# Optimization experiments

Hardware: AMD Instinct MI355X
Metric: run time of the kernel (lower is better)

The kernel has to match this reference:

```python
import jax, jax.numpy as jnp
import numpy as np
import math

DIMS = [2048, 1024, 512, 4096]
NH, DK, DV = 16, 64, 64
BS = 8192
D_MODEL = NH * DK  # 1024


def setup_inputs() -> dict:
    key = jax.random.key(0)
    ks = jax.random.split(key, 3 * len(DIMS) + 5)
    inp = {"input_data": jax.random.normal(ks[0], (BS, sum(DIMS)), jnp.float32)}
    ki = 1
    for i, d in enumerate(DIMS):
        inp[f"wq{i}"] = jax.random.normal(ks[ki], (NH * DK, d), jnp.float32) * 0.02; ki += 1
        inp[f"wk{i}"] = jax.random.normal(ks[ki], (NH * DK, d), jnp.float32) * 0.02; ki += 1
        inp[f"wv{i}"] = jax.random.normal(ks[ki], (NH * DV, d), jnp.float32) * 0.02; ki += 1
    inp["fc_w"] = jax.random.normal(ks[ki], (NH * DV, NH * DV), jnp.float32) * 0.02; ki += 1
    inp["fc_b"] = jax.random.normal(ks[ki], (NH * DV,), jnp.float32) * 0.02; ki += 1
    inp["ln_g"] = jnp.ones((NH * DV,), jnp.float32)
    inp["ln_b"] = jnp.zeros((NH * DV,), jnp.float32)
    return inp


def _forward(input_data, wqs, wks, wvs, fc_w, fc_b, ln_g, ln_b):
    bs = input_data.shape[0]
    M = len(DIMS)
    offs = np.cumsum([0] + DIMS)
    # per-modality projections; stack into [bs, M, NH*D]
    xs = [input_data[:, offs[i]:offs[i + 1]] for i in range(M)]
    q = jnp.stack([x @ w.T for x, w in zip(xs, wqs)], axis=1)  # [bs, M, NH*DK]
    k = jnp.stack([x @ w.T for x, w in zip(xs, wks)], axis=1)
    v = jnp.stack([x @ w.T for x, w in zip(xs, wvs)], axis=1)  # [bs, M, NH*DV]
    residual = v  # v.transpose(1,2).view == original stacked v
    qh = q.reshape(bs, M, NH, DK).transpose(0, 2, 1, 3)  # [bs, NH, M, DK]
    kh = k.reshape(bs, M, NH, DK).transpose(0, 2, 1, 3)
    vh = v.reshape(bs, M, NH, DV).transpose(0, 2, 1, 3)
    scores = jnp.einsum('bhqd,bhkd->bhqk', qh, kh) / math.sqrt(DK)
    attn = jax.nn.softmax(scores, axis=-1)  # [bs, NH, M, M]
    ctx = jnp.einsum('bhqk,bhkd->bhqd', attn, vh)  # [bs, NH, M, DV]
    ctx = ctx.transpose(0, 2, 1, 3).reshape(bs, M, NH * DV)
    out = ctx @ fc_w.T + fc_b  # dropout is identity (p=0 / eval)
    out = out + residual
    mu = jnp.mean(out, axis=-1, keepdims=True)
    var = jnp.var(out, axis=-1, keepdims=True)
    out = (out - mu) / jnp.sqrt(var + 1e-6) * ln_g + ln_b
    return out, attn


def reference(input_data, wq0, wk0, wv0, wq1, wk1, wv1, wq2, wk2, wv2,
              wq3, wk3, wv3, fc_w, fc_b, ln_g, ln_b):
    wqs = [wq0, wq1, wq2, wq3]
    wks = [wk0, wk1, wk2, wk3]
    wvs = [wv0, wv1, wv2, wv3]
    return _forward(input_data, wqs, wks, wvs, fc_w, fc_b, ln_g, ln_b)
```

## Files before the change

### kernel.cpp

```cpp
#include <hip/hip_runtime.h>


typedef unsigned short u16;
typedef short short8 __attribute__((ext_vector_type(8)));
typedef float f32x4 __attribute__((ext_vector_type(4)));

__device__ __forceinline__ u16 f2bf(float f) {
  unsigned u = __builtin_bit_cast(unsigned, f);
  u += 0x7FFFu + ((u >> 16) & 1u);
  return (u16)(u >> 16);
}
__device__ __forceinline__ float bf2f(u16 s) {
  return __builtin_bit_cast(float, ((unsigned)s) << 16);
}

__device__ __forceinline__ void gload16(const u16* g, u16* l) {
  __builtin_amdgcn_global_load_lds(
      (const __attribute__((address_space(1))) void*)g,
      (__attribute__((address_space(3))) void*)l, 16, 0, 0);
}

#define CFENCE asm volatile("" ::: "memory")

struct CArgs {
  const float* src[14];
  unsigned long dst[14];
  int blk0[14];
  int n4[14];
};

__global__ __launch_bounds__(256) void convall(CArgs a, u16* __restrict__ wsb) {
  int blk = blockIdx.x;
  int s = 0;
#pragma unroll
  for (int i = 1; i < 14; ++i) s = (blk >= a.blk0[i]) ? i : s;
  int li = (blk - a.blk0[s]) * 256 + threadIdx.x;
  if (li < a.n4[s]) {
    float4 v = ((const float4*)a.src[s])[li];
    ushort4 o;
    o.x = f2bf(v.x); o.y = f2bf(v.y); o.z = f2bf(v.z); o.w = f2bf(v.w);
    ((ushort4*)(wsb + a.dst[s]))[li] = o;
  }
}

template <int MODE>
__global__ __launch_bounds__(512, 2)
void gemm8(const u16* __restrict__ Abase, int lda,
           const u16* __restrict__ Wbase, u16* __restrict__ Cq,
           u16* __restrict__ Cpre, const float* __restrict__ bias,
           const u16* __restrict__ resid) {
  __shared__ __align__(16) u16 lds[65536];

  const int tid = threadIdx.x;
  const int w = tid >> 6, lane = tid & 63;
  const int lr = lane & 15, lk = lane >> 4;
  const int wm = w >> 2, wn = w & 3;

  int K, nt, bx, by, coff;
  const u16 *A, *B;
  if (MODE == 0) {
    int seg = blockIdx.x / 384;
    int r = blockIdx.x % 384;
    bx = r % 12; by = r / 12;
    K = 4096 >> seg; nt = 64 >> seg;
    int xo, wo, mod;
    switch (seg) {
      case 0:  xo = 3584; wo = 11010048; mod = 3; break;
      case 1:  xo = 0;    wo = 0;        mod = 0; break;
      case 2:  xo = 2048; wo = 6291456;  mod = 1; break;
      default: xo = 3072; wo = 9437184;  mod = 2; break;
    }
    coff = mod * 3072;
    A = Abase + xo;
    B = Wbase + wo;
  } else {
    bx = blockIdx.x & 3; by = blockIdx.x >> 2;
    K = 1024; nt = 16; coff = 0;
    A = Abase; B = Wbase;
  }
  const size_t brow = (size_t)by * 256;
  const int bcol = bx * 256;
  const u16* Ab = A + brow * (size_t)lda;
  const u16* Bb = B + (size_t)bcol * (size_t)K;

  f32x4 acc[8][4];
#pragma unroll
  for (int i = 0; i < 8; ++i)
#pragma unroll
    for (int j = 0; j < 4; ++j) acc[i][j] = (f32x4){0.f, 0.f, 0.f, 0.f};

  auto stageA = [&](int p, int half) {
    const int base = (p & 1) * 65536 + half * 16384;
    const int k0 = p * 64;
#pragma unroll
    for (int l = 0; l < 2; ++l) {
      int s = l * 8192 + tid * 16;
      int rw = s >> 7;
      int ck = ((s >> 4) & 7) ^ (rw & 7);
      int row = (rw & 63) + ((rw >> 6) << 7) + half * 64;
      gload16(Ab + (size_t)row * lda + k0 + ck * 8, &lds[(base + s) >> 1]);
    }
  };
  auto stageB = [&](int p, int half) {
    const int base = (p & 1) * 65536 + 32768 + half * 16384;
    const int k0 = p * 64;
#pragma unroll
    for (int l = 0; l < 2; ++l) {
      int s = l * 8192 + tid * 16;
      int rw = s >> 7;
      int ck = ((s >> 4) & 7) ^ (rw & 7);
      int col = (rw & 31) + ((rw >> 5) << 6) + half * 32;
      gload16(Bb + (size_t)col * (size_t)K + k0 + ck * 8, &lds[(base + s) >> 1]);
    }
  };

  auto ldA = [&](int t, int half, short8* dst) {
    const u16* lp = lds + (((t & 1) * 65536 + half * 16384) >> 1);
#pragma unroll
    for (int mi = 0; mi < 4; ++mi) {
      int rw = mi * 16 + lr + wm * 64;
#pragma unroll
      for (int ks = 0; ks < 2; ++ks) {
        int pc = (ks * 4 + lk) ^ (rw & 7);
        dst[mi * 2 + ks] = *(const short8*)(lp + rw * 64 + pc * 8);
      }
    }
  };
  auto ldB = [&](int t, int half, short8* dst) {
    const u16* lp = lds + (((t & 1) * 65536 + 32768 + half * 16384) >> 1);
#pragma unroll
    for (int ni = 0; ni < 2; ++ni) {
      int rw = ni * 16 + lr + wn * 32;
#pragma unroll
      for (int ks = 0; ks < 2; ++ks) {
        int pc = (ks * 4 + lk) ^ (rw & 7);
        dst[ni * 2 + ks] = *(const short8*)(lp + rw * 64 + pc * 8);
      }
    }
  };

  short8 af[8], bl[4], bh[4];
  auto MQ = [&](short8* a, short8* b, int mo, int no) {
#pragma unroll
    for (int mi = 0; mi < 4; ++mi)
#pragma unroll
      for (int ni = 0; ni < 2; ++ni) {
        acc[mo + mi][no + ni] = __builtin_amdgcn_mfma_f32_16x16x32_bf16(
            a[mi * 2 + 0], b[ni * 2 + 0], acc[mo + mi][no + ni], 0, 0, 0);
        acc[mo + mi][no + ni] = __builtin_amdgcn_mfma_f32_16x16x32_bf16(
            a[mi * 2 + 1], b[ni * 2 + 1], acc[mo + mi][no + ni], 0, 0, 0);
      }
  };

  stageA(0, 0); stageB(0, 0); stageB(0, 1); stageA(0, 1);
  asm volatile("s_waitcnt vmcnt(4)" ::: "memory");
  __builtin_amdgcn_s_barrier();
  CFENCE;

#pragma unroll 1
  for (int t = 0; t < nt; ++t) {
    const bool more = (t + 1 < nt);
    ldA(t, 0, af);
    ldB(t, 0, bl);
    if (more) stageA(t + 1, 0);
    CFENCE;
    __builtin_amdgcn_s_barrier();
    asm volatile("s_waitcnt lgkmcnt(0)" ::: "memory");
    __builtin_amdgcn_sched_barrier(0);
    __builtin_amdgcn_s_setprio(1);
    MQ(af, bl, 0, 0);
    __builtin_amdgcn_s_setprio(0);
    CFENCE;
    if (more) asm volatile("s_waitcnt vmcnt(4)" ::: "memory");
    else      asm volatile("s_waitcnt vmcnt(2)" ::: "memory");
    __builtin_amdgcn_s_barrier();
    CFENCE;
    ldB(t, 1, bh);
    if (more) stageB(t + 1, 0);
    CFENCE;
    __builtin_amdgcn_s_barrier();
    asm volatile("s_waitcnt lgkmcnt(0)" ::: "memory");
    __builtin_amdgcn_sched_barrier(0);
    __builtin_amdgcn_s_setprio(1);
    MQ(af, bh, 0, 2);
    __builtin_amdgcn_s_setprio(0);
    CFENCE;
    if (more) asm volatile("s_waitcnt vmcnt(4)" ::: "memory");
    else      asm volatile("s_waitcnt vmcnt(0)" ::: "memory");
    __builtin_amdgcn_s_barrier();
    CFENCE;
    ldA(t, 1, af);
    if (more) stageB(t + 1, 1);
    CFENCE;
    __builtin_amdgcn_s_barrier();
    asm volatile("s_waitcnt lgkmcnt(0)" ::: "memory");
    __builtin_amdgcn_sched_barrier(0);
    __builtin_amdgcn_s_setprio(1);
    MQ(af, bh, 4, 2);
    __builtin_amdgcn_s_setprio(0);
    CFENCE;
    __builtin_amdgcn_s_barrier();
    CFENCE;
    if (more) stageA(t + 1, 1);
    CFENCE;
    __builtin_amdgcn_s_barrier();
    __builtin_amdgcn_s_setprio(1);
    MQ(af, bl, 4, 0);
    __builtin_amdgcn_s_setprio(0);
    CFENCE;
    if (more) {
      asm volatile("s_waitcnt vmcnt(4)" ::: "memory");
      __builtin_amdgcn_s_barrier();
      CFENCE;
    }
  }

  if (MODE == 0) {
#pragma unroll
    for (int mi = 0; mi < 8; ++mi)
#pragma unroll
      for (int ni = 0; ni < 4; ++ni) {
        const int c = coff + bcol + wn * 64 + ni * 16 + lr;
#pragma unroll
        for (int j = 0; j < 4; ++j) {
          size_t r = brow + wm * 128 + mi * 16 + lk * 4 + j;
          Cq[r * 12288 + c] = f2bf(acc[mi][ni][j]);
        }
      }
  } else {
#pragma unroll
    for (int mi = 0; mi < 8; ++mi)
#pragma unroll
      for (int ni = 0; ni < 4; ++ni) {
        const int c = bcol + wn * 64 + ni * 16 + lr;
        const float bs = bias[c];
#pragma unroll
        for (int j = 0; j < 4; ++j) {
          size_t r = brow + wm * 128 + mi * 16 + lk * 4 + j;
          size_t ridx = (r >> 2) * 12288 + (r & 3) * 3072 + 2048 + c;
          Cpre[r * 1024 + c] = f2bf(acc[mi][ni][j] + bs + bf2f(resid[ridx]));
        }
      }
  }
}

__global__ __launch_bounds__(256) void attn_k(const u16* __restrict__ qkv,
                                              u16* __restrict__ ctxb,
                                              float* __restrict__ attn_out) {
  const int tid = threadIdx.x;
  const int l = tid & 63;
  const int wg = blockIdx.x * 4 + (tid >> 6);
  const int b = wg >> 2;
  const int h0 = (wg & 3) << 2;
  const size_t base = (size_t)b * 12288 + h0 * 64 + l * 4;

  float q[4][4], k[4][4], v[4][4];
#pragma unroll
  for (int m = 0; m < 4; ++m) {
    ushort4 uq = *(const ushort4*)(qkv + base + m * 3072);
    ushort4 uk = *(const ushort4*)(qkv + base + m * 3072 + 1024);
    ushort4 uv = *(const ushort4*)(qkv + base + m * 3072 + 2048);
    q[m][0] = bf2f(uq.x); q[m][1] = bf2f(uq.y); q[m][2] = bf2f(uq.z); q[m][3] = bf2f(uq.w);
    k[m][0] = bf2f(uk.x); k[m][1] = bf2f(uk.y); k[m][2] = bf2f(uk.z); k[m][3] = bf2f(uk.w);
    v[m][0] = bf2f(uv.x); v[m][1] = bf2f(uv.y); v[m][2] = bf2f(uv.z); v[m][3] = bf2f(uv.w);
  }

  float s[16];
#pragma unroll
  for (int i = 0; i < 4; ++i)
#pragma unroll
    for (int j = 0; j < 4; ++j) {
      float acc = q[i][0] * k[j][0];
      acc += q[i][1] * k[j][1];
      acc += q[i][2] * k[j][2];
      acc += q[i][3] * k[j][3];
      s[i * 4 + j] = acc;
    }
#pragma unroll
  for (int off = 1; off < 16; off <<= 1) {
#pragma unroll
    for (int t = 0; t < 16; ++t) s[t] += __shfl_xor(s[t], off);
  }

  float a[16];
#pragma unroll
  for (int i = 0; i < 4; ++i) {
    float s0 = s[i * 4 + 0] * 0.125f, s1 = s[i * 4 + 1] * 0.125f;
    float s2 = s[i * 4 + 2] * 0.125f, s3 = s[i * 4 + 3] * 0.125f;
    float m = fmaxf(fmaxf(s0, s1), fmaxf(s2, s3));
    float e0 = __expf(s0 - m), e1 = __expf(s1 - m);
    float e2 = __expf(s2 - m), e3 = __expf(s3 - m);
    float inv = 1.0f / (e0 + e1 + e2 + e3);
    a[i * 4 + 0] = e0 * inv; a[i * 4 + 1] = e1 * inv;
    a[i * 4 + 2] = e2 * inv; a[i * 4 + 3] = e3 * inv;
  }

#pragma unroll
  for (int i = 0; i < 4; ++i) {
    float c0 = a[i*4+0]*v[0][0] + a[i*4+1]*v[1][0] + a[i*4+2]*v[2][0] + a[i*4+3]*v[3][0];
    float c1 = a[i*4+0]*v[0][1] + a[i*4+1]*v[1][1] + a[i*4+2]*v[2][1] + a[i*4+3]*v[3][1];
    float c2 = a[i*4+0]*v[0][2] + a[i*4+1]*v[1][2] + a[i*4+2]*v[2][2] + a[i*4+3]*v[3][2];
    float c3 = a[i*4+0]*v[0][3] + a[i*4+1]*v[1][3] + a[i*4+2]*v[2][3] + a[i*4+3]*v[3][3];
    ushort4 o;
    o.x = f2bf(c0); o.y = f2bf(c1); o.z = f2bf(c2); o.w = f2bf(c3);
    *(ushort4*)(ctxb + (size_t)b * 4096 + i * 1024 + h0 * 64 + l * 4) = o;
  }

  int sel = l & 15;
  float val = a[0];
#pragma unroll
  for (int t = 1; t < 16; ++t) val = (sel == t) ? a[t] : val;
  attn_out[(size_t)b * 256 + h0 * 16 + l] = val;
}

__global__ __launch_bounds__(256) void ln_k(const u16* __restrict__ pre,
                                            const float* __restrict__ g,
                                            const float* __restrict__ b,
                                            float* __restrict__ out) {
  int row = blockIdx.x;
  int tid = threadIdx.x;
  ushort4 u = *(const ushort4*)(pre + (size_t)row * 1024 + tid * 4);
  float x0 = bf2f(u.x), x1 = bf2f(u.y), x2 = bf2f(u.z), x3 = bf2f(u.w);
  float s = x0 + x1 + x2 + x3;
  float s2 = x0 * x0 + x1 * x1 + x2 * x2 + x3 * x3;
#pragma unroll
  for (int off = 32; off; off >>= 1) {
    s += __shfl_xor(s, off);
    s2 += __shfl_xor(s2, off);
  }
  __shared__ float r1[4], r2[4];
  int w = tid >> 6, lane = tid & 63;
  if (lane == 0) { r1[w] = s; r2[w] = s2; }
  __syncthreads();
  s = r1[0] + r1[1] + r1[2] + r1[3];
  s2 = r2[0] + r2[1] + r2[2] + r2[3];
  float mu = s * (1.0f / 1024.0f);
  float inv = rsqrtf(s2 * (1.0f / 1024.0f) - mu * mu + 1e-6f);
  float4 gv = *(const float4*)(g + tid * 4);
  float4 bv = *(const float4*)(b + tid * 4);
  float4 o;
  o.x = (x0 - mu) * inv * gv.x + bv.x;
  o.y = (x1 - mu) * inv * gv.y + bv.y;
  o.z = (x2 - mu) * inv * gv.z + bv.z;
  o.w = (x3 - mu) * inv * gv.w + bv.w;
  *(float4*)(out + (size_t)row * 1024 + tid * 4) = o;
}

extern "C" void kernel_launch(void* const* d_in, const int* in_sizes, int n_in,
                              void* d_out, int out_size, void* d_ws,
                              size_t ws_size, hipStream_t stream) {
  const float* fcb = (const float*)d_in[14];
  const float* lng = (const float*)d_in[15];
  const float* lnb = (const float*)d_in[16];

  u16* wsb = (u16*)d_ws;
  u16* xb = wsb;
  u16* wb = xb + 62914560;
  u16* qkv = wb + 24641536;
  u16* ctxb = qkv + 100663296;
  u16* pre = wsb;
  float* outp = (float*)d_out;
  float* attn_out = outp + 33554432;

  static const unsigned long woff[13] = {
      0,        2097152,  4194304,
      6291456,  7340032,  8388608,
      9437184,  9961472,  10485760,
      11010048, 15204352, 19398656,
      23592960};
  static const int wn4[13] = {524288, 524288, 524288, 262144, 262144, 262144,
                              131072, 131072, 131072, 1048576, 1048576, 1048576,
                              262144};

  CArgs ca;
  ca.src[0] = (const float*)d_in[0];
  ca.dst[0] = 0;
  ca.n4[0] = 62914560 / 4;
  ca.blk0[0] = 0;
  int nb = ca.n4[0] / 256;
  for (int i = 0; i < 13; ++i) {
    ca.src[i + 1] = (const float*)d_in[1 + i];
    ca.dst[i + 1] = 62914560ul + woff[i];
    ca.n4[i + 1] = wn4[i];
    ca.blk0[i + 1] = nb;
    nb += (wn4[i] + 255) / 256;
  }
  convall<<<dim3(nb), 256, 0, stream>>>(ca, wsb);

  gemm8<0><<<dim3(1536), 512, 0, stream>>>(xb, 7680, wb, qkv, nullptr, nullptr,
                                           nullptr);

  attn_k<<<dim3(8192), 256, 0, stream>>>(qkv, ctxb, attn_out);

  gemm8<1><<<dim3(512), 512, 0, stream>>>(ctxb, 1024, wb + 23592960, nullptr,
                                          pre, fcb, qkv);

  ln_k<<<dim3(32768), 256, 0, stream>>>(pre, lng, lnb, outp);
}
```

Baseline: 617.0 us.

## Use nontemporal loads/stores in streaming kernels and regroup GEMM prefetch stages

Streaming accesses in the conversion, attention and layernorm kernels become nontemporal loads and stores so single-use data does not pollute the caches. The GEMM main loop now issues the next tile's A and B prefetches in two grouped batches instead of four separate points. This removes one barrier and one wait per iteration. The regrouping changes how many loads are in flight at each vmcnt wait, so the wait counts may no longer match the outstanding loads, which risks reading LDS before it is filled.

After: 609.6 us. Within noise of the previous version (-1.2%).

```diff
diff --git a/kernel.cpp b/kernel.cpp
--- a/kernel.cpp
+++ b/kernel.cpp
@@ -3,6 +3,7 @@
 
 typedef unsigned short u16;
 typedef short short8 __attribute__((ext_vector_type(8)));
+typedef unsigned short u16x4 __attribute__((ext_vector_type(4)));
 typedef float f32x4 __attribute__((ext_vector_type(4)));
 
 __device__ __forceinline__ u16 f2bf(float f) {
@@ -36,10 +37,10 @@
   for (int i = 1; i < 14; ++i) s = (blk >= a.blk0[i]) ? i : s;
   int li = (blk - a.blk0[s]) * 256 + threadIdx.x;
   if (li < a.n4[s]) {
-    float4 v = ((const float4*)a.src[s])[li];
-    ushort4 o;
+    f32x4 v = __builtin_nontemporal_load((const f32x4*)a.src[s] + li);
+    u16x4 o;
     o.x = f2bf(v.x); o.y = f2bf(v.y); o.z = f2bf(v.z); o.w = f2bf(v.w);
-    ((ushort4*)(wsb + a.dst[s]))[li] = o;
+    *((u16x4*)(wsb + a.dst[s]) + li) = o;
   }
 }
 
@@ -118,7 +119,7 @@
     const u16* lp = lds + (((t & 1) * 65536 + half * 16384) >> 1);
 #pragma unroll
     for (int mi = 0; mi < 4; ++mi) {
-      int rw = mi * 16 + lr + wm * 64;
+      int rw = wm * 64 + mi * 16 + lr;
 #pragma unroll
       for (int ks = 0; ks < 2; ++ks) {
         int pc = (ks * 4 + lk) ^ (rw & 7);
@@ -130,7 +131,7 @@
     const u16* lp = lds + (((t & 1) * 65536 + 32768 + half * 16384) >> 1);
 #pragma unroll
     for (int ni = 0; ni < 2; ++ni) {
-      int rw = ni * 16 + lr + wn * 32;
+      int rw = wn * 32 + ni * 16 + lr;
 #pragma unroll
       for (int ks = 0; ks < 2; ++ks) {
         int pc = (ks * 4 + lk) ^ (rw & 7);
@@ -162,7 +163,7 @@
     const bool more = (t + 1 < nt);
     ldA(t, 0, af);
     ldB(t, 0, bl);
-    if (more) stageA(t + 1, 0);
+    if (more) { stageA(t + 1, 0); stageB(t + 1, 0); }
     CFENCE;
     __builtin_amdgcn_s_barrier();
     asm volatile("s_waitcnt lgkmcnt(0)" ::: "memory");
@@ -172,11 +173,10 @@
     __builtin_amdgcn_s_setprio(0);
     CFENCE;
     if (more) asm volatile("s_waitcnt vmcnt(4)" ::: "memory");
-    else      asm volatile("s_waitcnt vmcnt(2)" ::: "memory");
+    else      asm volatile("s_waitcnt vmcnt(0)" ::: "memory");
     __builtin_amdgcn_s_barrier();
     CFENCE;
     ldB(t, 1, bh);
-    if (more) stageB(t + 1, 0);
     CFENCE;
     __builtin_amdgcn_s_barrier();
     asm volatile("s_waitcnt lgkmcnt(0)" ::: "memory");
@@ -185,12 +185,10 @@
     MQ(af, bh, 0, 2);
     __builtin_amdgcn_s_setprio(0);
     CFENCE;
-    if (more) asm volatile("s_waitcnt vmcnt(4)" ::: "memory");
-    else      asm volatile("s_waitcnt vmcnt(0)" ::: "memory");
     __builtin_amdgcn_s_barrier();
     CFENCE;
     ldA(t, 1, af);
-    if (more) stageB(t + 1, 1);
+    if (more) { stageB(t + 1, 1); stageA(t + 1, 1); }
     CFENCE;
     __builtin_amdgcn_s_barrier();
     asm volatile("s_waitcnt lgkmcnt(0)" ::: "memory");
@@ -201,9 +199,6 @@
     CFENCE;
     __builtin_amdgcn_s_barrier();
     CFENCE;
-    if (more) stageA(t + 1, 1);
-    CFENCE;
-    __builtin_amdgcn_s_barrier();
     __builtin_amdgcn_s_setprio(1);
     MQ(af, bl, 4, 0);
     __builtin_amdgcn_s_setprio(0);
@@ -257,9 +252,9 @@
   float q[4][4], k[4][4], v[4][4];
 #pragma unroll
   for (int m = 0; m < 4; ++m) {
-    ushort4 uq = *(const ushort4*)(qkv + base + m * 3072);
-    ushort4 uk = *(const ushort4*)(qkv + base + m * 3072 + 1024);
-    ushort4 uv = *(const ushort4*)(qkv + base + m * 3072 + 2048);
+    u16x4 uq = __builtin_nontemporal_load((const u16x4*)(qkv + base + m * 3072));
+    u16x4 uk = __builtin_nontemporal_load((const u16x4*)(qkv + base + m * 3072 + 1024));
+    u16x4 uv = __builtin_nontemporal_load((const u16x4*)(qkv + base + m * 3072 + 2048));
     q[m][0] = bf2f(uq.x); q[m][1] = bf2f(uq.y); q[m][2] = bf2f(uq.z); q[m][3] = bf2f(uq.w);
     k[m][0] = bf2f(uk.x); k[m][1] = bf2f(uk.y); k[m][2] = bf2f(uk.z); k[m][3] = bf2f(uk.w);
     v[m][0] = bf2f(uv.x); v[m][1] = bf2f(uv.y); v[m][2] = bf2f(uv.z); v[m][3] = bf2f(uv.w);
@@ -301,16 +296,16 @@
     float c1 = a[i*4+0]*v[0][1] + a[i*4+1]*v[1][1] + a[i*4+2]*v[2][1] + a[i*4+3]*v[3][1];
     float c2 = a[i*4+0]*v[0][2] + a[i*4+1]*v[1][2] + a[i*4+2]*v[2][2] + a[i*4+3]*v[3][2];
     float c3 = a[i*4+0]*v[0][3] + a[i*4+1]*v[1][3] + a[i*4+2]*v[2][3] + a[i*4+3]*v[3][3];
-    ushort4 o;
+    u16x4 o;
     o.x = f2bf(c0); o.y = f2bf(c1); o.z = f2bf(c2); o.w = f2bf(c3);
-    *(ushort4*)(ctxb + (size_t)b * 4096 + i * 1024 + h0 * 64 + l * 4) = o;
+    *(u16x4*)(ctxb + (size_t)b * 4096 + i * 1024 + h0 * 64 + l * 4) = o;
   }
 
   int sel = l & 15;
   float val = a[0];
 #pragma unroll
   for (int t = 1; t < 16; ++t) val = (sel == t) ? a[t] : val;
-  attn_out[(size_t)b * 256 + h0 * 16 + l] = val;
+  __builtin_nontemporal_store(val, &attn_out[(size_t)b * 256 + h0 * 16 + l]);
 }
 
 __global__ __launch_bounds__(256) void ln_k(const u16* __restrict__ pre,
@@ -319,7 +314,8 @@
                                             float* __restrict__ out) {
   int row = blockIdx.x;
   int tid = threadIdx.x;
-  ushort4 u = *(const ushort4*)(pre + (size_t)row * 1024 + tid * 4);
+  u16x4 u = __builtin_nontemporal_load(
+      (const u16x4*)(pre + (size_t)row * 1024 + tid * 4));
   float x0 = bf2f(u.x), x1 = bf2f(u.y), x2 = bf2f(u.z), x3 = bf2f(u.w);
   float s = x0 + x1 + x2 + x3;
   float s2 = x0 * x0 + x1 * x1 + x2 * x2 + x3 * x3;
@@ -338,12 +334,12 @@
   float inv = rsqrtf(s2 * (1.0f / 1024.0f) - mu * mu + 1e-6f);
   float4 gv = *(const float4*)(g + tid * 4);
   float4 bv = *(const float4*)(b + tid * 4);
-  float4 o;
+  f32x4 o;
   o.x = (x0 - mu) * inv * gv.x + bv.x;
   o.y = (x1 - mu) * inv * gv.y + bv.y;
   o.z = (x2 - mu) * inv * gv.z + bv.z;
   o.w = (x3 - mu) * inv * gv.w + bv.w;
-  *(float4*)(out + (size_t)row * 1024 + tid * 4) = o;
+  __builtin_nontemporal_store(o, (f32x4*)(out + (size_t)row * 1024 + tid * 4));
 }
 
 extern "C" void kernel_launch(void* const* d_in, const int* in_sizes, int n_in,
```
